# Optimization experiments

Measured on AMD Instinct MI355X. Metric: run time of the kernel, lower is better.

## Reference

```python
import jax, jax.numpy as jnp
import numpy as np

N = 50000
E = 800000
F_IN = 128
HID = 64
HEADS = 4
NEG_SLOPE = 0.2  # PyG GATConv default negative_slope


def segment_softmax(e, dst, num_segments):
    # numerically stable softmax over edges grouped by destination node
    m = jax.ops.segment_max(e, dst, num_segments=num_segments)
    ex = jnp.exp(e - m[dst])
    s = jax.ops.segment_sum(ex, dst, num_segments=num_segments)
    return ex / (s[dst] + 1e-16)


def gat_conv(x, src, dst, W, a_src, a_dst, bias, heads, out_ch, concat):
    n = x.shape[0]
    h = (x @ W).reshape(n, heads, out_ch)          # [N,H,C]
    alpha_s = (h * a_src).sum(-1)                  # [N,H]
    alpha_d = (h * a_dst).sum(-1)                  # [N,H]
    e = jax.nn.leaky_relu(alpha_s[src] + alpha_d[dst], NEG_SLOPE)  # [E,H]
    alpha = segment_softmax(e, dst, n)             # [E,H]
    out = jax.ops.segment_sum(h[src] * alpha[:, :, None], dst, num_segments=n)  # [N,H,C]
    out = out.reshape(n, heads * out_ch) if concat else out.mean(axis=1)
    return out + bias


def setup_inputs() -> dict:
    key = jax.random.key(0)
    ks = jax.random.split(key, 16)

    def lin(k, i, o):
        return (jax.random.normal(k, (i, o), jnp.float32) / np.float32(np.sqrt(i)))

    def att(k, h, c):
        return jax.random.normal(k, (h, c), jnp.float32) * np.float32(0.1)

    x = jax.random.normal(ks[0], (N, F_IN), jnp.float32)
    edge_index = jax.random.randint(ks[1], (2, E), 0, N, dtype=jnp.int32)
    return {
        "x": x,
        "W_emb": lin(ks[2], F_IN, HID), "b_emb": jnp.zeros(HID, jnp.float32),
        "W0": lin(ks[3], HID, HEADS * HID), "as0": att(ks[4], HEADS, HID), "ad0": att(ks[5], HEADS, HID), "b0": jnp.zeros(HEADS * HID, jnp.float32),
        "W1": lin(ks[6], HEADS * HID, HEADS * HID), "as1": att(ks[7], HEADS, HID), "ad1": att(ks[8], HEADS, HID), "b1": jnp.zeros(HEADS * HID, jnp.float32),
        "W2": lin(ks[9], HEADS * HID, HID), "as2": att(ks[10], 1, HID), "ad2": att(ks[11], 1, HID), "b2": jnp.zeros(HID, jnp.float32),
        "Wo1": lin(ks[12], HID, HID // 2), "bo1": jnp.zeros(HID // 2, jnp.float32),
        "Wo2": lin(ks[13], HID // 2, 1), "bo2": jnp.zeros(1, jnp.float32),
        "edge_index": edge_index,
    }


def reference(x, W_emb, b_emb, W0, as0, ad0, b0, W1, as1, ad1, b1, W2, as2, ad2, b2, Wo1, bo1, Wo2, bo2, edge_index):
    n = x.shape[0]
    loop = jnp.arange(n, dtype=edge_index.dtype)  # PyG GATConv adds self-loops
    src = jnp.concatenate([edge_index[0], loop])
    dst = jnp.concatenate([edge_index[1], loop])
    h = jax.nn.relu(x @ W_emb + b_emb)
    h = jax.nn.relu(gat_conv(h, src, dst, W0, as0, ad0, b0, HEADS, HID, True))   # dropout=identity (eval)
    h = jax.nn.relu(gat_conv(h, src, dst, W1, as1, ad1, b1, HEADS, HID, True))
    h = gat_conv(h, src, dst, W2, as2, ad2, b2, 1, HID, False)
    h = jax.nn.relu(h @ Wo1 + bo1)
    return h @ Wo2 + bo2  # [N,1]
```

## Files before the change

### kernel.cpp

```cpp
#include <hip/hip_runtime.h>

typedef _Float16 h8_t __attribute__((ext_vector_type(8)));
typedef _Float16 h4_t __attribute__((ext_vector_type(4)));
typedef float floatx4 __attribute__((ext_vector_type(4)));

__device__ __forceinline__ float leaky(float v) { return v >= 0.f ? v : 0.2f * v; }

__global__ void hist_kernel(const int* __restrict__ dst, int E, int* __restrict__ cnt) {
    int e = blockIdx.x * blockDim.x + threadIdx.x;
    if (e < E) atomicAdd(&cnt[dst[e]], 1);
}

__global__ __launch_bounds__(256) void blocksum_kernel(const int* __restrict__ cnt, int N,
                                                       int* __restrict__ bsum) {
    __shared__ int red[256];
    int tid = threadIdx.x;
    int idx = blockIdx.x * 256 + tid;
    red[tid] = idx < N ? cnt[idx] + 1 : 0;
    __syncthreads();
#pragma unroll
    for (int off = 128; off >= 1; off >>= 1) {
        if (tid < off) red[tid] += red[tid + off];
        __syncthreads();
    }
    if (tid == 0) bsum[blockIdx.x] = red[0];
}

__global__ __launch_bounds__(256) void scanbsum_kernel(int* __restrict__ bsum, int nb,
                                                       int* __restrict__ total) {
    __shared__ int part[256];
    int tid = threadIdx.x;
    int per = (nb + 255) / 256;
    int s0 = tid * per, s1 = min(s0 + per, nb);
    int s = 0;
    for (int i = s0; i < s1; i++) s += bsum[i];
    part[tid] = s;
    __syncthreads();
    for (int off = 1; off < 256; off <<= 1) {
        int v = (tid >= off) ? part[tid - off] : 0;
        __syncthreads();
        part[tid] += v;
        __syncthreads();
    }
    int base = (tid == 0) ? 0 : part[tid - 1];
    for (int i = s0; i < s1; i++) {
        int v = bsum[i];
        bsum[i] = base;
        base += v;
    }
    if (tid == 255) *total = part[255];
}

__global__ __launch_bounds__(256) void rowptr_kernel(const int* __restrict__ cnt,
                                                     const int* __restrict__ bsum, int N,
                                                     int* __restrict__ row_ptr,
                                                     int* __restrict__ cursor) {
    __shared__ int lds[256];
    int tid = threadIdx.x;
    int idx = blockIdx.x * 256 + tid;
    int v = idx < N ? cnt[idx] + 1 : 0;
    lds[tid] = v;
    __syncthreads();
    for (int off = 1; off < 256; off <<= 1) {
        int t = (tid >= off) ? lds[tid - off] : 0;
        __syncthreads();
        lds[tid] += t;
        __syncthreads();
    }
    if (idx < N) {
        int p = bsum[blockIdx.x] + lds[tid] - v;
        row_ptr[idx] = p;
        cursor[idx] = p;
    }
}

__global__ void scatter_kernel(const int* __restrict__ src, const int* __restrict__ dst,
                               int E, int N, int* __restrict__ cursor, int* __restrict__ csr_src) {
    int e = blockIdx.x * blockDim.x + threadIdx.x;
    if (e >= E + N) return;
    int s, d;
    if (e < E) { s = src[e]; d = dst[e]; }
    else       { s = e - E;  d = s; }
    int pos = atomicAdd(&cursor[d], 1);
    csr_src[pos] = s;
}

__global__ void prep_weights_all(const float* __restrict__ W_emb, const float* __restrict__ W0,
                                 const float* __restrict__ W1, const float* __restrict__ W2,
                                 _Float16* __restrict__ WeH, _Float16* __restrict__ WeL,
                                 _Float16* __restrict__ W0H, _Float16* __restrict__ W0L,
                                 _Float16* __restrict__ W1H, _Float16* __restrict__ W1L,
                                 _Float16* __restrict__ W2H, _Float16* __restrict__ W2L) {
    int which = blockIdx.y;
    const float* W;
    _Float16 *Wh, *Wl;
    int K, N;
    if (which == 0)      { W = W_emb; Wh = WeH; Wl = WeL; K = 128; N = 64; }
    else if (which == 1) { W = W0;    Wh = W0H; Wl = W0L; K = 64;  N = 256; }
    else if (which == 2) { W = W1;    Wh = W1H; Wl = W1L; K = 256; N = 256; }
    else                 { W = W2;    Wh = W2H; Wl = W2L; K = 256; N = 64; }
    int idx = blockIdx.x * blockDim.x + threadIdx.x;
    if (idx >= K * N) return;
    int k = idx / N, n = idx % N;
    float v = W[idx];
    _Float16 hi = (_Float16)v;
    _Float16 lo = (_Float16)(v - (float)hi);
    size_t o = ((size_t)(k >> 3) * N + n) * 8 + (k & 7);
    Wh[o] = hi; Wl[o] = lo;
}

__global__ __launch_bounds__(256) void gemm_emb_kernel(
        const float* __restrict__ X,
        const _Float16* __restrict__ Bh, const _Float16* __restrict__ Bl,
        const float* __restrict__ bias,
        _Float16* __restrict__ Ph, _Float16* __restrict__ Pl,
        int Mpad, int M) {
    const int Nn = 64, K = 128;
    __shared__ _Float16 Bs[2][16][64][8];
    __shared__ _Float16 stH[4][16][72];
    __shared__ _Float16 stL[4][16][72];
    int tid = threadIdx.x;
    int wv = tid >> 6, lane = tid & 63;
    int m16 = lane & 15, quad = lane >> 4;
    int row0 = blockIdx.x * 128 + wv * 32;

#pragma unroll
    for (int cc = 0; cc < 8; cc++) {
        int c = tid + cc * 256;
        int plane = c >> 10, rem = c & 1023, q = rem >> 6, col = rem & 63;
        const _Float16* srcp = (plane ? Bl : Bh) + ((size_t)q * Nn + col) * 8;
        *reinterpret_cast<h8_t*>(&Bs[plane][q][col][0]) = *reinterpret_cast<const h8_t*>(srcp);
    }
    __syncthreads();

    floatx4 acc[2][4];
#pragma unroll
    for (int t = 0; t < 2; t++)
#pragma unroll
        for (int c = 0; c < 4; c++)
#pragma unroll
            for (int i = 0; i < 4; i++) acc[t][c][i] = 0.f;

    int r0 = row0 + m16, r1 = row0 + 16 + m16;
#pragma unroll
    for (int kt4 = 0; kt4 < 4; kt4++) {
        int kcol = kt4 * 32 + quad * 8;
        float vs0[8] = {0,0,0,0,0,0,0,0}, vs1[8] = {0,0,0,0,0,0,0,0};
        if (r0 < M) {
            const float4* p = (const float4*)(X + (size_t)r0 * K + kcol);
            float4 a = p[0], b = p[1];
            vs0[0]=a.x; vs0[1]=a.y; vs0[2]=a.z; vs0[3]=a.w;
            vs0[4]=b.x; vs0[5]=b.y; vs0[6]=b.z; vs0[7]=b.w;
        }
        if (r1 < M) {
            const float4* p = (const float4*)(X + (size_t)r1 * K + kcol);
            float4 a = p[0], b = p[1];
            vs1[0]=a.x; vs1[1]=a.y; vs1[2]=a.z; vs1[3]=a.w;
            vs1[4]=b.x; vs1[5]=b.y; vs1[6]=b.z; vs1[7]=b.w;
        }
        h8_t ah0, al0, ah1, al1;
#pragma unroll
        for (int j = 0; j < 8; j++) {
            _Float16 hi0 = (_Float16)vs0[j];
            ah0[j] = hi0; al0[j] = (_Float16)(vs0[j] - (float)hi0);
            _Float16 hi1 = (_Float16)vs1[j];
            ah1[j] = hi1; al1[j] = (_Float16)(vs1[j] - (float)hi1);
        }
        int kq = kt4 * 4 + quad;
#pragma unroll
        for (int c = 0; c < 4; c++) {
            h8_t bh = *reinterpret_cast<const h8_t*>(&Bs[0][kq][c * 16 + m16][0]);
            h8_t bl = *reinterpret_cast<const h8_t*>(&Bs[1][kq][c * 16 + m16][0]);
            acc[0][c] = __builtin_amdgcn_mfma_f32_16x16x32_f16(ah0, bh, acc[0][c], 0, 0, 0);
            acc[1][c] = __builtin_amdgcn_mfma_f32_16x16x32_f16(ah1, bh, acc[1][c], 0, 0, 0);
            acc[0][c] = __builtin_amdgcn_mfma_f32_16x16x32_f16(ah0, bl, acc[0][c], 0, 0, 0);
            acc[1][c] = __builtin_amdgcn_mfma_f32_16x16x32_f16(ah1, bl, acc[1][c], 0, 0, 0);
            acc[0][c] = __builtin_amdgcn_mfma_f32_16x16x32_f16(al0, bh, acc[0][c], 0, 0, 0);
            acc[1][c] = __builtin_amdgcn_mfma_f32_16x16x32_f16(al1, bh, acc[1][c], 0, 0, 0);
        }
    }

#pragma unroll
    for (int t = 0; t < 2; t++) {
#pragma unroll
        for (int c = 0; c < 4; c++) {
            float bv = bias[c * 16 + m16];
#pragma unroll
            for (int i = 0; i < 4; i++) {
                float v = fmaxf(acc[t][c][i] + bv, 0.f);
                _Float16 hi = (_Float16)v;
                stH[wv][quad * 4 + i][c * 16 + m16] = hi;
                stL[wv][quad * 4 + i][c * 16 + m16] = (_Float16)(v - (float)hi);
            }
        }
        int rowChunk = row0 + t * 16;
#pragma unroll
        for (int it = 0; it < 2; it++) {
            int lid = it * 64 + lane;
            int kg = lid >> 4, rloc = lid & 15;
            h8_t vh = *reinterpret_cast<const h8_t*>(&stH[wv][rloc][kg * 8]);
            h8_t vl = *reinterpret_cast<const h8_t*>(&stL[wv][rloc][kg * 8]);
            size_t o = ((size_t)kg * Mpad + rowChunk + rloc) * 8;
            *reinterpret_cast<h8_t*>(Ph + o) = vh;
            *reinterpret_cast<h8_t*>(Pl + o) = vl;
        }
    }
}

__global__ __launch_bounds__(256) void gemm_gat0_kernel(
        const _Float16* __restrict__ Ah, const _Float16* __restrict__ Al,
        const _Float16* __restrict__ Bh, const _Float16* __restrict__ Bl,
        const float* __restrict__ a_src, const float* __restrict__ a_dst,
        _Float16* __restrict__ hOut, float* __restrict__ aS, float* __restrict__ aD,
        int Mpad, int M) {
    const int Nn = 256;
    __shared__ _Float16 Bs[2][8][128][8];
    __shared__ _Float16 st[4][16][136];
    int tid = threadIdx.x;
    int wv = tid >> 6, lane = tid & 63;
    int m16 = lane & 15, quad = lane >> 4;
    int row0 = blockIdx.x * 128 + wv * 32;
    int colBase = blockIdx.y * 128;
    size_t kqbase = (size_t)colBase * 8;

#pragma unroll
    for (int cc = 0; cc < 8; cc++) {
        int c = tid + cc * 256;
        int plane = c >> 10, rem = c & 1023, q = rem >> 7, col = rem & 127;
        const _Float16* srcp = (plane ? Bl : Bh) + kqbase + ((size_t)q * Nn + col) * 8;
        *reinterpret_cast<h8_t*>(&Bs[plane][q][col][0]) = *reinterpret_cast<const h8_t*>(srcp);
    }
    __syncthreads();

    floatx4 acc[2][8];
#pragma unroll
    for (int t = 0; t < 2; t++)
#pragma unroll
        for (int c = 0; c < 8; c++)
#pragma unroll
            for (int i = 0; i < 4; i++) acc[t][c][i] = 0.f;

#pragma unroll
    for (int kt = 0; kt < 2; kt++) {
        int kq = kt * 4 + quad;
        size_t aoff = ((size_t)kq * Mpad + row0 + m16) * 8;
        h8_t ah0 = *reinterpret_cast<const h8_t*>(Ah + aoff);
        h8_t ah1 = *reinterpret_cast<const h8_t*>(Ah + aoff + 128);
        h8_t al0 = *reinterpret_cast<const h8_t*>(Al + aoff);
        h8_t al1 = *reinterpret_cast<const h8_t*>(Al + aoff + 128);
#pragma unroll
        for (int c = 0; c < 8; c++) {
            h8_t bh = *reinterpret_cast<const h8_t*>(&Bs[0][kq][c * 16 + m16][0]);
            h8_t bl = *reinterpret_cast<const h8_t*>(&Bs[1][kq][c * 16 + m16][0]);
            acc[0][c] = __builtin_amdgcn_mfma_f32_16x16x32_f16(ah0, bh, acc[0][c], 0, 0, 0);
            acc[1][c] = __builtin_amdgcn_mfma_f32_16x16x32_f16(ah1, bh, acc[1][c], 0, 0, 0);
            acc[0][c] = __builtin_amdgcn_mfma_f32_16x16x32_f16(ah0, bl, acc[0][c], 0, 0, 0);
            acc[1][c] = __builtin_amdgcn_mfma_f32_16x16x32_f16(ah1, bl, acc[1][c], 0, 0, 0);
            acc[0][c] = __builtin_amdgcn_mfma_f32_16x16x32_f16(al0, bh, acc[0][c], 0, 0, 0);
            acc[1][c] = __builtin_amdgcn_mfma_f32_16x16x32_f16(al1, bh, acc[1][c], 0, 0, 0);
        }
    }

    float asv[8], adv[8];
#pragma unroll
    for (int c = 0; c < 8; c++) {
        asv[c] = a_src[colBase + c * 16 + m16];
        adv[c] = a_dst[colBase + c * 16 + m16];
    }
    int hb = colBase >> 6;
#pragma unroll
    for (int t = 0; t < 2; t++) {
#pragma unroll
        for (int i = 0; i < 4; i++) {
            int r = row0 + t * 16 + quad * 4 + i;
            float s0 = 0.f, d0 = 0.f, s1 = 0.f, d1 = 0.f;
#pragma unroll
            for (int c = 0; c < 8; c++) {
                float v = acc[t][c][i];
                if (c < 4) { s0 += v * asv[c]; d0 += v * adv[c]; }
                else       { s1 += v * asv[c]; d1 += v * adv[c]; }
            }
#pragma unroll
            for (int off = 1; off < 16; off <<= 1) {
                s0 += __shfl_xor(s0, off);
                d0 += __shfl_xor(d0, off);
                s1 += __shfl_xor(s1, off);
                d1 += __shfl_xor(d1, off);
            }
            if (m16 == 0 && r < M) {
                aS[r * 4 + hb] = s0;     aD[r * 4 + hb] = d0;
                aS[r * 4 + hb + 1] = s1; aD[r * 4 + hb + 1] = d1;
            }
        }
    }

#pragma unroll
    for (int t = 0; t < 2; t++) {
#pragma unroll
        for (int c = 0; c < 8; c++)
#pragma unroll
            for (int i = 0; i < 4; i++)
                st[wv][quad * 4 + i][c * 16 + m16] = (_Float16)acc[t][c][i];
        int rowChunk = row0 + t * 16;
#pragma unroll
        for (int it = 0; it < 4; it++) {
            int lid = it * 64 + lane;
            int rloc = lid >> 4, u = lid & 15;
            h8_t v = *reinterpret_cast<const h8_t*>(&st[wv][rloc][u * 8]);
            *reinterpret_cast<h8_t*>(hOut + (size_t)(rowChunk + rloc) * 256 + colBase + u * 8) = v;
        }
    }
}

__global__ __launch_bounds__(256) void gemm_gat1_kernel(
        const _Float16* __restrict__ Ah, const _Float16* __restrict__ Al,
        const _Float16* __restrict__ Bh, const _Float16* __restrict__ Bl,
        const float* __restrict__ a_src, const float* __restrict__ a_dst,
        _Float16* __restrict__ hOut, float* __restrict__ aS, float* __restrict__ aD,
        int Mpad, int M, int K) {
    const int Nn = 256;
    __shared__ _Float16 Bs[2][4][128][8];
    __shared__ _Float16 st[4][16][136];
    int tid = threadIdx.x;
    int wv = tid >> 6, lane = tid & 63;
    int m16 = lane & 15, quad = lane >> 4;
    int row0 = blockIdx.x * 128 + wv * 32;
    int colBase = blockIdx.y * 128;

    floatx4 acc[2][8];
#pragma unroll
    for (int t = 0; t < 2; t++)
#pragma unroll
        for (int c = 0; c < 8; c++)
#pragma unroll
            for (int i = 0; i < 4; i++) acc[t][c][i] = 0.f;

    int sPlane[4], sQ[4], sCol[4];
    const _Float16* sBase[4];
#pragma unroll
    for (int cc = 0; cc < 4; cc++) {
        int c = tid + cc * 256;
        sPlane[cc] = c >> 9;
        int rem = c & 511;
        sQ[cc] = rem >> 7;
        sCol[cc] = rem & 127;
        sBase[cc] = (sPlane[cc] ? Bl : Bh) + ((size_t)sQ[cc] * Nn + sCol[cc]) * 8;
    }

    size_t aoff = ((size_t)quad * Mpad + row0 + m16) * 8;
    size_t kqbase = (size_t)colBase * 8;
    const size_t aStep = (size_t)Mpad * 32;
    const size_t bStep = (size_t)Nn * 32;

    h8_t aR[4], bR[4];
    aR[0] = *reinterpret_cast<const h8_t*>(Ah + aoff);
    aR[1] = *reinterpret_cast<const h8_t*>(Ah + aoff + 128);
    aR[2] = *reinterpret_cast<const h8_t*>(Al + aoff);
    aR[3] = *reinterpret_cast<const h8_t*>(Al + aoff + 128);
#pragma unroll
    for (int cc = 0; cc < 4; cc++)
        bR[cc] = *reinterpret_cast<const h8_t*>(sBase[cc] + kqbase);

    for (int kt = 0; kt < K; kt += 32) {
#pragma unroll
        for (int cc = 0; cc < 4; cc++)
            *reinterpret_cast<h8_t*>(&Bs[sPlane[cc]][sQ[cc]][sCol[cc]][0]) = bR[cc];
        __syncthreads();
        h8_t aN[4], bN[4];
        bool more = (kt + 32) < K;
        if (more) {
            aoff += aStep; kqbase += bStep;
            aN[0] = *reinterpret_cast<const h8_t*>(Ah + aoff);
            aN[1] = *reinterpret_cast<const h8_t*>(Ah + aoff + 128);
            aN[2] = *reinterpret_cast<const h8_t*>(Al + aoff);
            aN[3] = *reinterpret_cast<const h8_t*>(Al + aoff + 128);
#pragma unroll
            for (int cc = 0; cc < 4; cc++)
                bN[cc] = *reinterpret_cast<const h8_t*>(sBase[cc] + kqbase);
        }
#pragma unroll
        for (int c = 0; c < 8; c++) {
            h8_t bh = *reinterpret_cast<const h8_t*>(&Bs[0][quad][c * 16 + m16][0]);
            h8_t bl = *reinterpret_cast<const h8_t*>(&Bs[1][quad][c * 16 + m16][0]);
            acc[0][c] = __builtin_amdgcn_mfma_f32_16x16x32_f16(aR[0], bh, acc[0][c], 0, 0, 0);
            acc[1][c] = __builtin_amdgcn_mfma_f32_16x16x32_f16(aR[1], bh, acc[1][c], 0, 0, 0);
            acc[0][c] = __builtin_amdgcn_mfma_f32_16x16x32_f16(aR[0], bl, acc[0][c], 0, 0, 0);
            acc[1][c] = __builtin_amdgcn_mfma_f32_16x16x32_f16(aR[1], bl, acc[1][c], 0, 0, 0);
            acc[0][c] = __builtin_amdgcn_mfma_f32_16x16x32_f16(aR[2], bh, acc[0][c], 0, 0, 0);
            acc[1][c] = __builtin_amdgcn_mfma_f32_16x16x32_f16(aR[3], bh, acc[1][c], 0, 0, 0);
        }
        __syncthreads();
        if (more) {
#pragma unroll
            for (int j = 0; j < 4; j++) { aR[j] = aN[j]; bR[j] = bN[j]; }
        }
    }

    float asv[8], adv[8];
#pragma unroll
    for (int c = 0; c < 8; c++) {
        asv[c] = a_src[colBase + c * 16 + m16];
        adv[c] = a_dst[colBase + c * 16 + m16];
    }
    int hb = colBase >> 6;
#pragma unroll
    for (int t = 0; t < 2; t++) {
#pragma unroll
        for (int i = 0; i < 4; i++) {
            int r = row0 + t * 16 + quad * 4 + i;
            float s0 = 0.f, d0 = 0.f, s1 = 0.f, d1 = 0.f;
#pragma unroll
            for (int c = 0; c < 8; c++) {
                float v = acc[t][c][i];
                if (c < 4) { s0 += v * asv[c]; d0 += v * adv[c]; }
                else       { s1 += v * asv[c]; d1 += v * adv[c]; }
            }
#pragma unroll
            for (int off = 1; off < 16; off <<= 1) {
                s0 += __shfl_xor(s0, off);
                d0 += __shfl_xor(d0, off);
                s1 += __shfl_xor(s1, off);
                d1 += __shfl_xor(d1, off);
            }
            if (m16 == 0 && r < M) {
                aS[r * 4 + hb] = s0;     aD[r * 4 + hb] = d0;
                aS[r * 4 + hb + 1] = s1; aD[r * 4 + hb + 1] = d1;
            }
        }
    }

#pragma unroll
    for (int t = 0; t < 2; t++) {
#pragma unroll
        for (int c = 0; c < 8; c++)
#pragma unroll
            for (int i = 0; i < 4; i++)
                st[wv][quad * 4 + i][c * 16 + m16] = (_Float16)acc[t][c][i];
        int rowChunk = row0 + t * 16;
#pragma unroll
        for (int it = 0; it < 4; it++) {
            int lid = it * 64 + lane;
            int rloc = lid >> 4, u = lid & 15;
            h8_t v = *reinterpret_cast<const h8_t*>(&st[wv][rloc][u * 8]);
            *reinterpret_cast<h8_t*>(hOut + (size_t)(rowChunk + rloc) * 256 + colBase + u * 8) = v;
        }
    }
}

__global__ __launch_bounds__(256) void gemm_l2_kernel(
        const _Float16* __restrict__ Ah, const _Float16* __restrict__ Al,
        const _Float16* __restrict__ Bh, const _Float16* __restrict__ Bl,
        const float* __restrict__ a_src, const float* __restrict__ a_dst,
        _Float16* __restrict__ hOut, float* __restrict__ aS, float* __restrict__ aD,
        int Mpad, int M, int K) {
    const int Nn = 64;
    __shared__ _Float16 Bs[2][4][64][8];
    __shared__ _Float16 st[4][16][72];
    int tid = threadIdx.x;
    int wv = tid >> 6, lane = tid & 63;
    int m16 = lane & 15, quad = lane >> 4;
    int row0 = blockIdx.x * 128 + wv * 32;

    floatx4 acc[2][4];
#pragma unroll
    for (int t = 0; t < 2; t++)
#pragma unroll
        for (int c = 0; c < 4; c++)
#pragma unroll
            for (int i = 0; i < 4; i++) acc[t][c][i] = 0.f;

    int sPlane[2], sQ[2], sCol[2];
    const _Float16* sBase[2];
#pragma unroll
    for (int cc = 0; cc < 2; cc++) {
        int c = tid + cc * 256;
        sPlane[cc] = c >> 8;
        int rem = c & 255;
        sQ[cc] = rem >> 6;
        sCol[cc] = rem & 63;
        sBase[cc] = (sPlane[cc] ? Bl : Bh) + ((size_t)sQ[cc] * Nn + sCol[cc]) * 8;
    }

    size_t aoff = ((size_t)quad * Mpad + row0 + m16) * 8;
    size_t kqbase = 0;
    const size_t aStep = (size_t)Mpad * 32;
    const size_t bStep = (size_t)Nn * 32;

    h8_t aR[4], bR[2];
    aR[0] = *reinterpret_cast<const h8_t*>(Ah + aoff);
    aR[1] = *reinterpret_cast<const h8_t*>(Ah + aoff + 128);
    aR[2] = *reinterpret_cast<const h8_t*>(Al + aoff);
    aR[3] = *reinterpret_cast<const h8_t*>(Al + aoff + 128);
#pragma unroll
    for (int cc = 0; cc < 2; cc++)
        bR[cc] = *reinterpret_cast<const h8_t*>(sBase[cc] + kqbase);

    for (int kt = 0; kt < K; kt += 32) {
#pragma unroll
        for (int cc = 0; cc < 2; cc++)
            *reinterpret_cast<h8_t*>(&Bs[sPlane[cc]][sQ[cc]][sCol[cc]][0]) = bR[cc];
        __syncthreads();
        h8_t aN[4], bN[2];
        bool more = (kt + 32) < K;
        if (more) {
            aoff += aStep; kqbase += bStep;
            aN[0] = *reinterpret_cast<const h8_t*>(Ah + aoff);
            aN[1] = *reinterpret_cast<const h8_t*>(Ah + aoff + 128);
            aN[2] = *reinterpret_cast<const h8_t*>(Al + aoff);
            aN[3] = *reinterpret_cast<const h8_t*>(Al + aoff + 128);
#pragma unroll
            for (int cc = 0; cc < 2; cc++)
                bN[cc] = *reinterpret_cast<const h8_t*>(sBase[cc] + kqbase);
        }
#pragma unroll
        for (int c = 0; c < 4; c++) {
            h8_t bh = *reinterpret_cast<const h8_t*>(&Bs[0][quad][c * 16 + m16][0]);
            h8_t bl = *reinterpret_cast<const h8_t*>(&Bs[1][quad][c * 16 + m16][0]);
            acc[0][c] = __builtin_amdgcn_mfma_f32_16x16x32_f16(aR[0], bh, acc[0][c], 0, 0, 0);
            acc[1][c] = __builtin_amdgcn_mfma_f32_16x16x32_f16(aR[1], bh, acc[1][c], 0, 0, 0);
            acc[0][c] = __builtin_amdgcn_mfma_f32_16x16x32_f16(aR[0], bl, acc[0][c], 0, 0, 0);
            acc[1][c] = __builtin_amdgcn_mfma_f32_16x16x32_f16(aR[1], bl, acc[1][c], 0, 0, 0);
            acc[0][c] = __builtin_amdgcn_mfma_f32_16x16x32_f16(aR[2], bh, acc[0][c], 0, 0, 0);
            acc[1][c] = __builtin_amdgcn_mfma_f32_16x16x32_f16(aR[3], bh, acc[1][c], 0, 0, 0);
        }
        __syncthreads();
        if (more) {
            aR[0] = aN[0]; aR[1] = aN[1]; aR[2] = aN[2]; aR[3] = aN[3];
            bR[0] = bN[0]; bR[1] = bN[1];
        }
    }

    float asv[4], adv[4];
#pragma unroll
    for (int c = 0; c < 4; c++) {
        asv[c] = a_src[c * 16 + m16];
        adv[c] = a_dst[c * 16 + m16];
    }
#pragma unroll
    for (int t = 0; t < 2; t++) {
#pragma unroll
        for (int i = 0; i < 4; i++) {
            int r = row0 + t * 16 + quad * 4 + i;
            float s0 = 0.f, d0 = 0.f;
#pragma unroll
            for (int c = 0; c < 4; c++) {
                float v = acc[t][c][i];
                s0 += v * asv[c]; d0 += v * adv[c];
            }
#pragma unroll
            for (int off = 1; off < 16; off <<= 1) {
                s0 += __shfl_xor(s0, off);
                d0 += __shfl_xor(d0, off);
            }
            if (m16 == 0 && r < M) { aS[r] = s0; aD[r] = d0; }
        }
    }

#pragma unroll
    for (int t = 0; t < 2; t++) {
#pragma unroll
        for (int c = 0; c < 4; c++)
#pragma unroll
            for (int i = 0; i < 4; i++)
                st[wv][quad * 4 + i][c * 16 + m16] = (_Float16)acc[t][c][i];
        int rowChunk = row0 + t * 16;
#pragma unroll
        for (int it = 0; it < 2; it++) {
            int lid = it * 64 + lane;
            int rloc = lid >> 3, u = lid & 7;
            h8_t v = *reinterpret_cast<const h8_t*>(&st[wv][rloc][u * 8]);
            *reinterpret_cast<h8_t*>(hOut + (size_t)(rowChunk + rloc) * 64 + u * 8) = v;
        }
    }
}

template <int TAG>
__global__ __launch_bounds__(256) void aggregate4_kernel(const _Float16* __restrict__ hsrc,
                                                         const float* __restrict__ alpha_s,
                                                         const float* __restrict__ alpha_d,
                                                         const int* __restrict__ row_ptr,
                                                         const int* __restrict__ csr_src,
                                                         const float* __restrict__ bias,
                                                         _Float16* __restrict__ outH,
                                                         _Float16* __restrict__ outL,
                                                         int N, int Mpad) {
    __shared__ float wlds[4][64][4];
    __shared__ int   slds[4][64];
    int wv = threadIdx.x >> 6, lane = threadIdx.x & 63;
    int node = blockIdx.x * 4 + wv;
    if (node >= N) return;
    int rs = row_ptr[node], re = row_ptr[node + 1];
    int slot = lane >> 5, lp = lane & 31;
    int ghead = lp >> 3;
    int gbyte = lp * 16;
    float4 ad4 = *(const float4*)(alpha_d + (size_t)node * 4);

    float den0 = 0.f, den1 = 0.f, den2 = 0.f, den3 = 0.f;
    float acc8[8] = {0.f, 0.f, 0.f, 0.f, 0.f, 0.f, 0.f, 0.f};
    float* wp = &wlds[wv][0][0];
    int*   sp = &slds[wv][0];
    const char* hbase = (const char*)hsrc;
    for (int base = rs; base < re; base += 64) {
        int i = base + lane;
        float w0 = 0.f, w1 = 0.f, w2 = 0.f, w3 = 0.f;
        int off = 0;
        if (i < re) {
            int s = csr_src[i];
            float4 as = *(const float4*)(alpha_s + (size_t)s * 4);
            w0 = __expf(fminf(leaky(as.x + ad4.x), 60.f));
            w1 = __expf(fminf(leaky(as.y + ad4.y), 60.f));
            w2 = __expf(fminf(leaky(as.z + ad4.z), 60.f));
            w3 = __expf(fminf(leaky(as.w + ad4.w), 60.f));
            off = s * 512;
        }
        den0 += w0; den1 += w1; den2 += w2; den3 += w3;
        sp[lane] = off;
        *(float4*)(wp + lane * 4) = make_float4(w0, w1, w2, w3);
        int cnt = min(64, re - base);
#pragma unroll 2
        for (int j = slot; j < cnt; j += 2) {
            int o2 = sp[j];
            float w = wp[j * 4 + ghead];
            h8_t hv = *reinterpret_cast<const h8_t*>(hbase + o2 + gbyte);
#pragma unroll
            for (int k = 0; k < 8; k++) acc8[k] += w * (float)hv[k];
        }
    }
#pragma unroll
    for (int k = 0; k < 8; k++) acc8[k] += __shfl_xor(acc8[k], 32);
#pragma unroll
    for (int off = 32; off >= 1; off >>= 1) {
        den0 += __shfl_xor(den0, off);
        den1 += __shfl_xor(den1, off);
        den2 += __shfl_xor(den2, off);
        den3 += __shfl_xor(den3, off);
    }
    if (slot == 0) {
        float den = (ghead & 2) ? ((ghead & 1) ? den3 : den2) : ((ghead & 1) ? den1 : den0);
        float inv = 1.f / (den + 1e-16f);
        int cbase = lp * 8;
        float4 b0 = *(const float4*)(bias + cbase);
        float4 b1 = *(const float4*)(bias + cbase + 4);
        float bv[8] = {b0.x, b0.y, b0.z, b0.w, b1.x, b1.y, b1.z, b1.w};
        h8_t hv, lv;
#pragma unroll
        for (int k = 0; k < 8; k++) {
            float v = fmaxf(acc8[k] * inv + bv[k], 0.f);
            _Float16 hi = (_Float16)v;
            hv[k] = hi;
            lv[k] = (_Float16)(v - (float)hi);
        }
        size_t o = ((size_t)lp * Mpad + node) * 8;
        *reinterpret_cast<h8_t*>(outH + o) = hv;
        *reinterpret_cast<h8_t*>(outL + o) = lv;
    }
}

__global__ __launch_bounds__(256) void agg1_mlp_kernel(const _Float16* __restrict__ hsrc,
                                                       const float* __restrict__ alpha_s,
                                                       const float* __restrict__ alpha_d,
                                                       const int* __restrict__ row_ptr,
                                                       const int* __restrict__ csr_src,
                                                       const float* __restrict__ bias,
                                                       const float* __restrict__ Wo1,
                                                       const float* __restrict__ bo1,
                                                       const float* __restrict__ Wo2,
                                                       const float* __restrict__ bo2,
                                                       float* __restrict__ out, int N) {
    __shared__ float wlds[4][64];
    __shared__ int   slds[4][64];
    __shared__ float hrow[4][64];
    __shared__ float w1s[64 * 32];
    __shared__ float w2s[32];
    __shared__ float b1s[32];
    int tid = threadIdx.x;
#pragma unroll
    for (int i = 0; i < 8; i++) w1s[tid + i * 256] = Wo1[tid + i * 256];
    if (tid < 32) { w2s[tid] = Wo2[tid]; b1s[tid] = bo1[tid]; }
    __syncthreads();

    int wv = tid >> 6, lane = tid & 63;
    int node = blockIdx.x * 4 + wv;
    if (node >= N) return;
    int rs = row_ptr[node], re = row_ptr[node + 1];
    float ad = alpha_d[node];
    int slot = lane >> 3, lp = lane & 7;
    int gbyte = lp * 16;

    float den = 0.f;
    float acc8[8] = {0.f, 0.f, 0.f, 0.f, 0.f, 0.f, 0.f, 0.f};
    const char* hbase = (const char*)hsrc;
    float* wp = &wlds[wv][0];
    int*   sp = &slds[wv][0];
    for (int base = rs; base < re; base += 64) {
        int i = base + lane;
        float w = 0.f;
        int off = 0;
        if (i < re) {
            int s = csr_src[i];
            w = __expf(fminf(leaky(alpha_s[s] + ad), 60.f));
            off = s * 128;
        }
        den += w;
        sp[lane] = off;
        wp[lane] = w;
        int cnt = min(64, re - base);
#pragma unroll 2
        for (int j = slot; j < cnt; j += 8) {
            float wj = wp[j];
            h8_t hv = *reinterpret_cast<const h8_t*>(hbase + sp[j] + gbyte);
#pragma unroll
            for (int k = 0; k < 8; k++) acc8[k] += wj * (float)hv[k];
        }
    }
#pragma unroll
    for (int k = 0; k < 8; k++) {
        acc8[k] += __shfl_xor(acc8[k], 8);
        acc8[k] += __shfl_xor(acc8[k], 16);
        acc8[k] += __shfl_xor(acc8[k], 32);
    }
#pragma unroll
    for (int off = 32; off >= 1; off >>= 1) den += __shfl_xor(den, off);
    if (slot == 0) {
        float inv = 1.f / (den + 1e-16f);
        int cbase = lp * 8;
#pragma unroll
        for (int k = 0; k < 8; k++)
            hrow[wv][cbase + k] = acc8[k] * inv + bias[cbase + k];
    }
    int j = lane & 31;
    float a = b1s[j];
#pragma unroll 4
    for (int k = 0; k < 64; k++) a += hrow[wv][k] * w1s[k * 32 + j];
    a = fmaxf(a, 0.f);
    float p = a * w2s[j];
#pragma unroll
    for (int off = 16; off >= 1; off >>= 1) p += __shfl_xor(p, off);
    if (lane == 0) out[node] = p + bo2[0];
}

extern "C" void kernel_launch(void* const* d_in, const int* in_sizes, int n_in,
                              void* d_out, int out_size, void* d_ws, size_t ws_size,
                              hipStream_t stream) {
    const float* x     = (const float*)d_in[0];
    const float* W_emb = (const float*)d_in[1];
    const float* b_emb = (const float*)d_in[2];
    const float* W0    = (const float*)d_in[3];
    const float* as0   = (const float*)d_in[4];
    const float* ad0   = (const float*)d_in[5];
    const float* b0    = (const float*)d_in[6];
    const float* W1    = (const float*)d_in[7];
    const float* as1   = (const float*)d_in[8];
    const float* ad1   = (const float*)d_in[9];
    const float* b1    = (const float*)d_in[10];
    const float* W2    = (const float*)d_in[11];
    const float* as2   = (const float*)d_in[12];
    const float* ad2   = (const float*)d_in[13];
    const float* b2    = (const float*)d_in[14];
    const float* Wo1   = (const float*)d_in[15];
    const float* bo1   = (const float*)d_in[16];
    const float* Wo2   = (const float*)d_in[17];
    const float* bo2   = (const float*)d_in[18];
    const int* eidx    = (const int*)d_in[19];

    const int N = in_sizes[0] / 128;
    const int E = in_sizes[19] / 2;
    const int* esrc = eidx;
    const int* edst = eidx + E;
    const int gmB  = (N + 127) / 128;
    const int Mpad = gmB * 128;
    const int nb   = (N + 255) / 256;

    char* w = (char*)d_ws;
    auto alloc = [&](size_t bytes) {
        char* p = w;
        w += (bytes + 255) & ~(size_t)255;
        return (void*)p;
    };
    _Float16* hOut = (_Float16*)alloc((size_t)Mpad * 256 * 2);
    _Float16* PHh  = (_Float16*)alloc((size_t)Mpad * 256 * 2);
    _Float16* PHl  = (_Float16*)alloc((size_t)Mpad * 256 * 2);
    float* aS      = (float*)alloc((size_t)N * 4 * 4);
    float* aD      = (float*)alloc((size_t)N * 4 * 4);
    int*   row_ptr = (int*)alloc((size_t)(N + 1) * 4);
    int*   cursor  = (int*)alloc((size_t)N * 4);
    int*   cnt     = (int*)alloc((size_t)N * 4);
    int*   bsum    = (int*)alloc((size_t)nb * 4);
    int*   csr     = (int*)alloc((size_t)(E + N) * 4);
    _Float16* WeH  = (_Float16*)alloc(128 * 64 * 2);
    _Float16* WeL  = (_Float16*)alloc(128 * 64 * 2);
    _Float16* W0H  = (_Float16*)alloc(64 * 256 * 2);
    _Float16* W0L  = (_Float16*)alloc(64 * 256 * 2);
    _Float16* W1H  = (_Float16*)alloc(256 * 256 * 2);
    _Float16* W1L  = (_Float16*)alloc(256 * 256 * 2);
    _Float16* W2H  = (_Float16*)alloc(256 * 64 * 2);
    _Float16* W2L  = (_Float16*)alloc(256 * 64 * 2);

    hipMemsetAsync(cnt, 0, (size_t)N * 4, stream);
    hist_kernel<<<(E + 255) / 256, 256, 0, stream>>>(edst, E, cnt);
    blocksum_kernel<<<nb, 256, 0, stream>>>(cnt, N, bsum);
    scanbsum_kernel<<<1, 256, 0, stream>>>(bsum, nb, row_ptr + N);
    rowptr_kernel<<<nb, 256, 0, stream>>>(cnt, bsum, N, row_ptr, cursor);
    scatter_kernel<<<(E + N + 255) / 256, 256, 0, stream>>>(esrc, edst, E, N, cursor, csr);

    prep_weights_all<<<dim3(256, 4), 256, 0, stream>>>(W_emb, W0, W1, W2,
                                                       WeH, WeL, W0H, W0L, W1H, W1L, W2H, W2L);

    int gn4 = (N + 3) / 4;

    gemm_emb_kernel<<<dim3(gmB, 1), 256, 0, stream>>>(x, WeH, WeL, b_emb, PHh, PHl, Mpad, N);

    gemm_gat0_kernel<<<dim3(gmB, 2), 256, 0, stream>>>(PHh, PHl, W0H, W0L, as0, ad0, hOut, aS, aD, Mpad, N);
    aggregate4_kernel<0><<<gn4, 256, 0, stream>>>(hOut, aS, aD, row_ptr, csr, b0, PHh, PHl, N, Mpad);

    gemm_gat1_kernel<<<dim3(gmB, 2), 256, 0, stream>>>(PHh, PHl, W1H, W1L, as1, ad1, hOut, aS, aD, Mpad, N, 256);
    aggregate4_kernel<1><<<gn4, 256, 0, stream>>>(hOut, aS, aD, row_ptr, csr, b1, PHh, PHl, N, Mpad);

    gemm_l2_kernel<<<dim3(gmB, 1), 256, 0, stream>>>(PHh, PHl, W2H, W2L, as2, ad2, hOut, aS, aD, Mpad, N, 256);
    agg1_mlp_kernel<<<gn4, 256, 0, stream>>>(hOut, aS, aD, row_ptr, csr, b2,
                                             Wo1, bo1, Wo2, bo2, (float*)d_out, N);
}
```

Baseline: 481.3 us.

## Store GAT hidden features in 32-channel column groups and split aggregation per group

The two multi-head GEMMs now write h in a column-grouped layout (8 groups of 32 channels, each a contiguous [Mpad,32] slab) instead of row-major 256-wide rows. The aggregation kernel launches 8x more blocks, each handling one 32-channel group for 4 nodes. Each gathered row is then 64 bytes, served by 4 lanes per edge, with 16 edges processed in parallel per wave. This aims to improve cache locality per group and raise parallelism, but it recomputes the attention weights 8 times per edge (twice per head) and rereads the CSR 8 times. It also adds nontemporal loads and stores.

```diff
diff --git a/kernel.cpp b/kernel.cpp
--- a/kernel.cpp
+++ b/kernel.cpp
@@ -307,7 +307,9 @@
             int lid = it * 64 + lane;
             int rloc = lid >> 4, u = lid & 15;
             h8_t v = *reinterpret_cast<const h8_t*>(&st[wv][rloc][u * 8]);
-            *reinterpret_cast<h8_t*>(hOut + (size_t)(rowChunk + rloc) * 256 + colBase + u * 8) = v;
+            int col = colBase + u * 8;
+            int grp = col >> 5, c32 = col & 31;
+            *reinterpret_cast<h8_t*>(hOut + ((size_t)grp * Mpad + rowChunk + rloc) * 32 + c32) = v;
         }
     }
 }
@@ -442,7 +444,9 @@
             int lid = it * 64 + lane;
             int rloc = lid >> 4, u = lid & 15;
             h8_t v = *reinterpret_cast<const h8_t*>(&st[wv][rloc][u * 8]);
-            *reinterpret_cast<h8_t*>(hOut + (size_t)(rowChunk + rloc) * 256 + colBase + u * 8) = v;
+            int col = colBase + u * 8;
+            int grp = col >> 5, c32 = col & 31;
+            *reinterpret_cast<h8_t*>(hOut + ((size_t)grp * Mpad + rowChunk + rloc) * 32 + c32) = v;
         }
     }
 }
@@ -574,7 +578,6 @@
     }
 }
 
-template <int TAG>
 __global__ __launch_bounds__(256) void aggregate4_kernel(const _Float16* __restrict__ hsrc,
                                                          const float* __restrict__ alpha_s,
                                                          const float* __restrict__ alpha_d,
@@ -584,63 +587,56 @@
                                                          _Float16* __restrict__ outH,
                                                          _Float16* __restrict__ outL,
                                                          int N, int Mpad) {
-    __shared__ float wlds[4][64][4];
+    __shared__ float wlds[4][64];
     __shared__ int   slds[4][64];
-    int wv = threadIdx.x >> 6, lane = threadIdx.x & 63;
-    int node = blockIdx.x * 4 + wv;
+    int tid = threadIdx.x;
+    int wv = tid >> 6, lane = tid & 63;
+    int grp = blockIdx.x & 7;
+    int head = grp >> 1;
+    int node = (blockIdx.x >> 3) * 4 + wv;
     if (node >= N) return;
     int rs = row_ptr[node], re = row_ptr[node + 1];
-    int slot = lane >> 5, lp = lane & 31;
-    int ghead = lp >> 3;
-    int gbyte = lp * 16;
-    float4 ad4 = *(const float4*)(alpha_d + (size_t)node * 4);
-
-    float den0 = 0.f, den1 = 0.f, den2 = 0.f, den3 = 0.f;
+    int slot = lane >> 2, lp = lane & 3;
+    float adv = alpha_d[node * 4 + head];
+    const char* hbase = (const char*)hsrc + (size_t)grp * Mpad * 64;
+
+    float den = 0.f;
     float acc8[8] = {0.f, 0.f, 0.f, 0.f, 0.f, 0.f, 0.f, 0.f};
-    float* wp = &wlds[wv][0][0];
+    float* wp = &wlds[wv][0];
     int*   sp = &slds[wv][0];
-    const char* hbase = (const char*)hsrc;
     for (int base = rs; base < re; base += 64) {
         int i = base + lane;
-        float w0 = 0.f, w1 = 0.f, w2 = 0.f, w3 = 0.f;
-        int off = 0;
+        float w = 0.f;
+        int s = 0;
         if (i < re) {
-            int s = csr_src[i];
-            float4 as = *(const float4*)(alpha_s + (size_t)s * 4);
-            w0 = __expf(fminf(leaky(as.x + ad4.x), 60.f));
-            w1 = __expf(fminf(leaky(as.y + ad4.y), 60.f));
-            w2 = __expf(fminf(leaky(as.z + ad4.z), 60.f));
-            w3 = __expf(fminf(leaky(as.w + ad4.w), 60.f));
-            off = s * 512;
-        }
-        den0 += w0; den1 += w1; den2 += w2; den3 += w3;
-        sp[lane] = off;
-        *(float4*)(wp + lane * 4) = make_float4(w0, w1, w2, w3);
+            s = __builtin_nontemporal_load(csr_src + i);
+            w = __expf(fminf(leaky(alpha_s[s * 4 + head] + adv), 60.f));
+        }
+        den += w;
+        sp[lane] = s;
+        wp[lane] = w;
         int cnt = min(64, re - base);
-#pragma unroll 2
-        for (int j = slot; j < cnt; j += 2) {
-            int o2 = sp[j];
-            float w = wp[j * 4 + ghead];
-            h8_t hv = *reinterpret_cast<const h8_t*>(hbase + o2 + gbyte);
-#pragma unroll
-            for (int k = 0; k < 8; k++) acc8[k] += w * (float)hv[k];
-        }
-    }
-#pragma unroll
-    for (int k = 0; k < 8; k++) acc8[k] += __shfl_xor(acc8[k], 32);
-#pragma unroll
-    for (int off = 32; off >= 1; off >>= 1) {
-        den0 += __shfl_xor(den0, off);
-        den1 += __shfl_xor(den1, off);
-        den2 += __shfl_xor(den2, off);
-        den3 += __shfl_xor(den3, off);
-    }
+        for (int j = slot; j < cnt; j += 16) {
+            float wj = wp[j];
+            h8_t hv = *reinterpret_cast<const h8_t*>(hbase + (size_t)sp[j] * 64 + lp * 16);
+#pragma unroll
+            for (int k = 0; k < 8; k++) acc8[k] += wj * (float)hv[k];
+        }
+    }
+#pragma unroll
+    for (int k = 0; k < 8; k++) {
+        acc8[k] += __shfl_xor(acc8[k], 4);
+        acc8[k] += __shfl_xor(acc8[k], 8);
+        acc8[k] += __shfl_xor(acc8[k], 16);
+        acc8[k] += __shfl_xor(acc8[k], 32);
+    }
+#pragma unroll
+    for (int off = 32; off >= 1; off >>= 1) den += __shfl_xor(den, off);
     if (slot == 0) {
-        float den = (ghead & 2) ? ((ghead & 1) ? den3 : den2) : ((ghead & 1) ? den1 : den0);
         float inv = 1.f / (den + 1e-16f);
-        int cbase = lp * 8;
-        float4 b0 = *(const float4*)(bias + cbase);
-        float4 b1 = *(const float4*)(bias + cbase + 4);
+        int ch0 = grp * 32 + lp * 8;
+        float4 b0 = *(const float4*)(bias + ch0);
+        float4 b1 = *(const float4*)(bias + ch0 + 4);
         float bv[8] = {b0.x, b0.y, b0.z, b0.w, b1.x, b1.y, b1.z, b1.w};
         h8_t hv, lv;
 #pragma unroll
@@ -650,9 +646,10 @@
             hv[k] = hi;
             lv[k] = (_Float16)(v - (float)hi);
         }
-        size_t o = ((size_t)lp * Mpad + node) * 8;
-        *reinterpret_cast<h8_t*>(outH + o) = hv;
-        *reinterpret_cast<h8_t*>(outL + o) = lv;
+        int kq = grp * 4 + lp;
+        size_t o = ((size_t)kq * Mpad + node) * 8;
+        __builtin_nontemporal_store(hv, reinterpret_cast<h8_t*>(outH + o));
+        __builtin_nontemporal_store(lv, reinterpret_cast<h8_t*>(outL + o));
     }
 }
 
@@ -807,14 +804,15 @@
                                                        WeH, WeL, W0H, W0L, W1H, W1L, W2H, W2L);
 
     int gn4 = (N + 3) / 4;
+    int gnAgg = gn4 * 8;
 
     gemm_emb_kernel<<<dim3(gmB, 1), 256, 0, stream>>>(x, WeH, WeL, b_emb, PHh, PHl, Mpad, N);
 
     gemm_gat0_kernel<<<dim3(gmB, 2), 256, 0, stream>>>(PHh, PHl, W0H, W0L, as0, ad0, hOut, aS, aD, Mpad, N);
-    aggregate4_kernel<0><<<gn4, 256, 0, stream>>>(hOut, aS, aD, row_ptr, csr, b0, PHh, PHl, N, Mpad);
+    aggregate4_kernel<<<gnAgg, 256, 0, stream>>>(hOut, aS, aD, row_ptr, csr, b0, PHh, PHl, N, Mpad);
 
     gemm_gat1_kernel<<<dim3(gmB, 2), 256, 0, stream>>>(PHh, PHl, W1H, W1L, as1, ad1, hOut, aS, aD, Mpad, N, 256);
-    aggregate4_kernel<1><<<gn4, 256, 0, stream>>>(hOut, aS, aD, row_ptr, csr, b1, PHh, PHl, N, Mpad);
+    aggregate4_kernel<<<gnAgg, 256, 0, stream>>>(hOut, aS, aD, row_ptr, csr, b1, PHh, PHl, N, Mpad);
 
     gemm_l2_kernel<<<dim3(gmB, 1), 256, 0, stream>>>(PHh, PHl, W2H, W2L, as2, ad2, hOut, aS, aD, Mpad, N, 256);
     agg1_mlp_kernel<<<gn4, 256, 0, stream>>>(hOut, aS, aD, row_ptr, csr, b2,
```

Result: slower. 733.3 us (+52.4%).
